# Performance work log

Hardware: AMD Instinct MI355X
Metric: run time of the kernel (lower is better)

The kernel has to match this reference:

```python
import jax, jax.numpy as jnp
import numpy as np

N, F = 4096, 255          # nodes, raw feature dim (one-hot adds +1 -> 256)
HID, D = 256, 256         # GCN hidden and out_dim
B, T, G = 8, 16384, 4     # n_breakings, n_tuples, n_groups
LN_EPS = 1e-5


def setup_inputs() -> dict:
    key = jax.random.key(0)
    ks = jax.random.split(key, 8)
    X = jax.random.normal(ks[0], (N, F), jnp.float32)
    adj_t = jax.random.uniform(ks[1], (N, N), jnp.float32)  # dense weighted adjacency
    W1 = jax.random.normal(ks[2], (F + 1, HID), jnp.float32) * 0.05
    b1 = jnp.zeros((HID,), jnp.float32)
    W2 = jax.random.normal(ks[3], (HID, D), jnp.float32) * 0.05
    b2 = jnp.zeros((D,), jnp.float32)
    ln_gamma = jnp.ones((D,), jnp.float32)
    ln_beta = jnp.zeros((D,), jnp.float32)
    tuples_coo = jax.random.randint(ks[4], (2, T), 0, N)
    group_idx = jax.random.randint(ks[5], (B,), 0, G)
    return dict(X=X, adj_t=adj_t, W1=W1, b1=b1, W2=W2, b2=b2,
                ln_gamma=ln_gamma, ln_beta=ln_beta,
                tuples_coo=tuples_coo, group_idx=group_idx,
                n_breakings=B, n_groups=G)


def reference(X, adj_t, W1, b1, W2, b2, ln_gamma, ln_beta,
              tuples_coo, group_idx, n_breakings, n_groups):
    n = X.shape[0]
    # --- symmetry breaking: top-k degree nodes (ties improbable for float degrees) ---
    deg = adj_t.sum(-1)                                   # [N]
    _, brk_idx = jax.lax.top_k(deg, n_breakings)          # [B]
    one_hot = jax.nn.one_hot(brk_idx, n, dtype=X.dtype)   # [B, N]
    # --- concat broadcast features with one-hot breaking channel ---
    Xin = jnp.concatenate(
        [jnp.broadcast_to(X[None], (n_breakings,) + X.shape), one_hot[..., None]],
        axis=-1)                                          # [B, N, F+1]
    # --- symmetry_breaking_model: 2-layer dense-adjacency GCN ---
    h = jax.nn.relu(jnp.einsum('nm,bmf->bnf', adj_t, Xin) @ W1 + b1)   # [B, N, HID]
    out = jnp.einsum('nm,bmf->bnf', adj_t, h) @ W2 + b2                # [B, N, D]
    # --- LayerNorm over feature dim ---
    mu = out.mean(-1, keepdims=True)
    var = out.var(-1, keepdims=True)
    holo = (out - mu) * jax.lax.rsqrt(var + LN_EPS) * ln_gamma + ln_beta  # [B, N, D]
    # --- gather tuple endpoints and reduce by product over arity ---
    gathered = holo[:, tuples_coo]                        # [B, arity, T, D]
    set_repr = gathered.prod(axis=1)                      # [B, T, D]
    # --- scatter-mean over breakings by group ---
    sums = jax.ops.segment_sum(set_repr, group_idx, num_segments=n_groups)  # [G, T, D]
    counts = jax.ops.segment_sum(jnp.ones((set_repr.shape[0],), set_repr.dtype),
                                 group_idx, num_segments=n_groups)          # [G]
    link = sums / jnp.maximum(counts, 1.0)[:, None, None]  # [G, T, D]
    # transpose(0,1).flatten(1,2): [T, G*D]
    return jnp.transpose(link, (1, 0, 2)).reshape(link.shape[1], -1)
```

## Files before the change

### kernel.cpp

```cpp
#include <hip/hip_runtime.h>
#include <hip/hip_bf16.h>

#define N_NODES 4096
#define FEAT    255
#define NB      8
#define NT      16384
#define NG      4

typedef __attribute__((ext_vector_type(8))) short          short8;
typedef __attribute__((ext_vector_type(8))) __bf16         bf16x8;
typedef __attribute__((ext_vector_type(4))) float          f32x4;
typedef __attribute__((ext_vector_type(4))) unsigned short ushort4v;

__device__ __forceinline__ unsigned short f2bf(float f) {
  unsigned int u = __builtin_bit_cast(unsigned int, f);
  u += 0x7fffu + ((u >> 16) & 1u);
  return (unsigned short)(u >> 16);
}

__device__ __forceinline__ f32x4 mfma16(short8 a, short8 b, f32x4 c) {
  return __builtin_amdgcn_mfma_f32_16x16x32_bf16(
      __builtin_bit_cast(bf16x8, a), __builtin_bit_cast(bf16x8, b), c, 0, 0, 0);
}

__device__ __forceinline__ void gload_lds16(const void* g, void* l) {
  __builtin_amdgcn_global_load_lds((__attribute__((address_space(1))) void*)(void*)g,
                                   (__attribute__((address_space(3))) void*)l, 16, 0, 0);
}

__global__ __launch_bounds__(256)
void deg_cvt(const float* __restrict__ adj, unsigned short* __restrict__ adjbf,
             float* __restrict__ deg)
{
  const int n = blockIdx.x;
  const int tid = threadIdx.x;
  const float* row = adj + (size_t)n * N_NODES;
  float s = 0.f;
#pragma unroll
  for (int it = 0; it < 4; ++it) {
    int idx = it * 1024 + tid * 4;
    float4 v = *(const float4*)(row + idx);
    s += (v.x + v.y) + (v.z + v.w);
    ushort4v o;
    o[0] = f2bf(v.x); o[1] = f2bf(v.y); o[2] = f2bf(v.z); o[3] = f2bf(v.w);
    *(ushort4v*)(adjbf + (size_t)n * N_NODES + idx) = o;
  }
#pragma unroll
  for (int off = 32; off > 0; off >>= 1) s += __shfl_xor(s, off);
  __shared__ float ws4[4];
  if ((tid & 63) == 0) ws4[tid >> 6] = s;
  __syncthreads();
  if (tid == 0) deg[n] = (ws4[0] + ws4[1]) + (ws4[2] + ws4[3]);
}

__global__ __launch_bounds__(256)
void topk_kernel(const float* __restrict__ deg, int* __restrict__ brk)
{
  __shared__ float v[N_NODES];
  __shared__ float wv[4];
  __shared__ int   wi[4];
  const int tid = threadIdx.x;
  for (int i = tid; i < N_NODES; i += 256) v[i] = deg[i];
  __syncthreads();
  for (int it = 0; it < NB; ++it) {
    float best = -1e30f; int bidx = 0x7fffffff;
#pragma unroll
    for (int k = 0; k < N_NODES / 256; ++k) {
      int i = k * 256 + tid;
      float x = v[i];
      if (x > best) { best = x; bidx = i; }
    }
#pragma unroll
    for (int off = 1; off < 64; off <<= 1) {
      float ov = __shfl_xor(best, off);
      int   oi = __shfl_xor(bidx, off);
      if (ov > best || (ov == best && oi < bidx)) { best = ov; bidx = oi; }
    }
    if ((tid & 63) == 0) { wv[tid >> 6] = best; wi[tid >> 6] = bidx; }
    __syncthreads();
    if (tid == 0) {
      float bb = wv[0]; int bbi = wi[0];
#pragma unroll
      for (int k = 1; k < 4; ++k)
        if (wv[k] > bb || (wv[k] == bb && wi[k] < bbi)) { bb = wv[k]; bbi = wi[k]; }
      brk[it] = bbi;
      v[bbi] = -1e30f;
    }
    __syncthreads();
  }
}

__global__ __launch_bounds__(256)
void extract_cols(const float* __restrict__ adj, const int* __restrict__ brk,
                  float* __restrict__ adjcol)
{
  const int n = blockIdx.x * 256 + threadIdx.x;
#pragma unroll
  for (int b = 0; b < NB; ++b)
    adjcol[b * N_NODES + n] = adj[(size_t)n * N_NODES + brk[b]];
}

#define G0R 8
__global__ __launch_bounds__(256)
void gemm0(const float* __restrict__ X, const float* __restrict__ W1,
           unsigned short* __restrict__ Yt)
{
  __shared__ float xr[G0R][256];
  const int tid = threadIdx.x;
  const int m0  = blockIdx.x * G0R;
  for (int i = tid; i < G0R * FEAT; i += 256) {
    int r = i / FEAT, c = i - r * FEAT;
    xr[r][c] = X[(size_t)(m0 + r) * FEAT + c];
  }
  __syncthreads();
  const int d = tid;
  float s[G0R] = {};
  for (int fq = 0; fq < 252; fq += 4) {
    float w0 = W1[(fq + 0) * 256 + d];
    float w1 = W1[(fq + 1) * 256 + d];
    float w2 = W1[(fq + 2) * 256 + d];
    float w3 = W1[(fq + 3) * 256 + d];
#pragma unroll
    for (int r = 0; r < G0R; ++r) {
      float4 x4 = *(const float4*)&xr[r][fq];
      s[r] = fmaf(x4.x, w0, s[r]);
      s[r] = fmaf(x4.y, w1, s[r]);
      s[r] = fmaf(x4.z, w2, s[r]);
      s[r] = fmaf(x4.w, w3, s[r]);
    }
  }
  for (int f = 252; f < FEAT; ++f) {
    float wv = W1[f * 256 + d];
#pragma unroll
    for (int r = 0; r < G0R; ++r) s[r] = fmaf(xr[r][f], wv, s[r]);
  }
#pragma unroll
  for (int r = 0; r < G0R; ++r)
    Yt[(size_t)d * N_NODES + m0 + r] = f2bf(s[r]);
}

__global__ __launch_bounds__(256)
void w2t_kernel(const float* __restrict__ W2, unsigned short* __restrict__ W2t)
{
  const int k = blockIdx.x, d = threadIdx.x;
  W2t[(size_t)d * 256 + k] = f2bf(W2[(size_t)k * 256 + d]);
}

template<int BM, int BN, int BK, int FM, int FN, bool OUTBF>
__global__ __launch_bounds__(256)
void gemm_bt(const unsigned short* __restrict__ A, const unsigned short* __restrict__ Bt,
             void* __restrict__ Cv, int M, int Nn, int K)
{
  static_assert(BK == 64, "staging/swizzle math assumes BK=64 (128 B = 8 chunks/row)");
  __shared__ unsigned short As[BM * BK];
  __shared__ unsigned short Bs[BN * BK];
  const int tid  = threadIdx.x;
  const int lane = tid & 63;
  const int w    = tid >> 6;
  const int wr   = w >> 1, wc = w & 1;
  const int lhi  = lane >> 4, llo = lane & 15;
  const int brow = blockIdx.x * BM;
  const int bcol = blockIdx.y * BN;
  const int Kper = K / gridDim.z;
  const int kbeg = blockIdx.z * Kper;

  f32x4 acc[FM][FN];
  const f32x4 z = {0.f, 0.f, 0.f, 0.f};
#pragma unroll
  for (int m = 0; m < FM; ++m)
#pragma unroll
    for (int n = 0; n < FN; ++n) acc[m][n] = z;

  for (int k0 = kbeg; k0 < kbeg + Kper; k0 += BK) {
    __syncthreads();
#pragma unroll
    for (int i = 0; i < (BM * BK * 2) / 4096; ++i) {
      int byte = i * 4096 + tid * 16;
      int row  = byte >> 7;
      int sc   = ((byte >> 4) & 7) ^ (row & 7);
      gload_lds16(A + (size_t)(brow + row) * K + k0 + sc * 8,
                  As + ((i * 4096 + w * 1024) >> 1));
    }
#pragma unroll
    for (int i = 0; i < (BN * BK * 2) / 4096; ++i) {
      int byte = i * 4096 + tid * 16;
      int row  = byte >> 7;
      int sc   = ((byte >> 4) & 7) ^ (row & 7);
      gload_lds16(Bt + (size_t)(bcol + row) * K + k0 + sc * 8,
                  Bs + ((i * 4096 + w * 1024) >> 1));
    }
    __syncthreads();
#pragma unroll
    for (int kk = 0; kk < BK; kk += 32) {
      short8 fa[FM], fb[FN];
#pragma unroll
      for (int m = 0; m < FM; ++m) {
        const int ar = wr * FM * 16 + m * 16 + llo;
        const int ac = ((kk >> 3) + lhi) ^ (ar & 7);
        fa[m] = *(const short8*)&As[ar * BK + ac * 8];
      }
#pragma unroll
      for (int n = 0; n < FN; ++n) {
        const int br = wc * FN * 16 + n * 16 + llo;
        const int bc = ((kk >> 3) + lhi) ^ (br & 7);
        fb[n] = *(const short8*)&Bs[br * BK + bc * 8];
      }
#pragma unroll
      for (int m = 0; m < FM; ++m)
#pragma unroll
        for (int n = 0; n < FN; ++n)
          acc[m][n] = mfma16(fa[m], fb[n], acc[m][n]);
    }
  }
#pragma unroll
  for (int m = 0; m < FM; ++m)
#pragma unroll
    for (int n = 0; n < FN; ++n) {
      const int r = brow + wr * FM * 16 + m * 16 + lhi * 4;
      const int c = bcol + wc * FN * 16 + n * 16 + llo;
      if constexpr (OUTBF) {
        unsigned short* cp = (unsigned short*)Cv + (size_t)blockIdx.z * M * Nn
                             + (size_t)r * Nn + c;
#pragma unroll
        for (int i = 0; i < 4; ++i) cp[(size_t)i * Nn] = f2bf(acc[m][n][i]);
      } else {
        float* cp = (float*)Cv + (size_t)blockIdx.z * M * Nn + (size_t)r * Nn + c;
#pragma unroll
        for (int i = 0; i < 4; ++i) cp[(size_t)i * Nn] = acc[m][n][i];
      }
    }
}

__global__ __launch_bounds__(256)
void reduce4(const float* __restrict__ bp, float* __restrict__ base)
{
  const size_t i = (size_t)blockIdx.x * 256 + threadIdx.x;
  const float4* b0 = (const float4*)bp;
  const float4* b1 = b0 + (size_t)N_NODES * 256 / 4;
  const float4* b2 = b1 + (size_t)N_NODES * 256 / 4;
  const float4* b3 = b2 + (size_t)N_NODES * 256 / 4;
  float4 v0 = b0[i], v1 = b1[i], v2 = b2[i], v3 = b3[i];
  float4 o;
  o.x = ((v0.x + v1.x) + v2.x) + v3.x;
  o.y = ((v0.y + v1.y) + v2.y) + v3.y;
  o.z = ((v0.z + v1.z) + v2.z) + v3.z;
  o.w = ((v0.w + v1.w) + v2.w) + v3.w;
  ((float4*)base)[i] = o;
}

__global__ __launch_bounds__(256)
void h_kernel(const float* __restrict__ base, const float* __restrict__ adjcol,
              const float* __restrict__ b1, const float* __restrict__ W1,
              unsigned short* __restrict__ Ht)
{
  __shared__ float bs[32][261];
  const int tid = threadIdx.x;
  const int m0  = blockIdx.x * 32;
  const int b   = blockIdx.y;
#pragma unroll
  for (int it = 0; it < 8; ++it) {
    int lin = it * 1024 + tid * 4;
    int mm = lin >> 8, d = lin & 255;
    float4 v = *(const float4*)(base + (size_t)(m0 + mm) * 256 + d);
    bs[mm][d] = v.x; bs[mm][d + 1] = v.y; bs[mm][d + 2] = v.z; bs[mm][d + 3] = v.w;
  }
  __syncthreads();
  const int ml = tid & 31, dg = tid >> 5;
  const float ac = adjcol[b * N_NODES + m0 + ml];
  const float* w1l = W1 + 255 * 256;
#pragma unroll 4
  for (int dd = 0; dd < 32; ++dd) {
    int d = dg * 32 + dd;
    float v = bs[ml][d] + b1[d] + ac * w1l[d];
    v = fmaxf(v, 0.f);
    Ht[(size_t)(b * 256 + d) * N_NODES + m0 + ml] = f2bf(v);
  }
}

__global__ __launch_bounds__(256)
void gemm3_ln(const unsigned short* __restrict__ Mcat, const unsigned short* __restrict__ W2t,
              const float* __restrict__ b2, const float* __restrict__ gamma,
              const float* __restrict__ beta, float* __restrict__ holo)
{
  const int tid  = threadIdx.x;
  const int w    = tid >> 6, lane = tid & 63;
  const int lhi  = lane >> 4, llo = lane & 15;
  const int n0   = blockIdx.x * 64;
  const int b    = blockIdx.y;
  const int row0 = n0 + w * 16;

  f32x4 acc[16];
  const f32x4 z = {0.f, 0.f, 0.f, 0.f};
#pragma unroll
  for (int j = 0; j < 16; ++j) acc[j] = z;

  const unsigned short* arow = Mcat + (size_t)(row0 + llo) * 2048 + b * 256;
#pragma unroll
  for (int k0 = 0; k0 < 256; k0 += 32) {
    const short8 fa = *(const short8*)&arow[k0 + lhi * 8];
#pragma unroll
    for (int j = 0; j < 16; ++j) {
      const short8 fb = *(const short8*)&W2t[(size_t)(j * 16 + llo) * 256 + k0 + lhi * 8];
      acc[j] = mfma16(fa, fb, acc[j]);
    }
  }
  float b2v[16];
#pragma unroll
  for (int j = 0; j < 16; ++j) b2v[j] = b2[j * 16 + llo];

  float mu[4], rs[4];
#pragma unroll
  for (int i = 0; i < 4; ++i) {
    float s = 0.f;
#pragma unroll
    for (int j = 0; j < 16; ++j) s += acc[j][i] + b2v[j];
    s += __shfl_xor(s, 1); s += __shfl_xor(s, 2);
    s += __shfl_xor(s, 4); s += __shfl_xor(s, 8);
    mu[i] = s * (1.f / 256.f);
  }
#pragma unroll
  for (int i = 0; i < 4; ++i) {
    float q = 0.f;
#pragma unroll
    for (int j = 0; j < 16; ++j) { float d = acc[j][i] + b2v[j] - mu[i]; q += d * d; }
    q += __shfl_xor(q, 1); q += __shfl_xor(q, 2);
    q += __shfl_xor(q, 4); q += __shfl_xor(q, 8);
    rs[i] = rsqrtf(q * (1.f / 256.f) + 1e-5f);
  }
  float* hb = holo + ((size_t)b * N_NODES + row0 + lhi * 4) * 256 + llo;
#pragma unroll
  for (int j = 0; j < 16; ++j) {
    const float gv = gamma[j * 16 + llo];
    const float bt = beta[j * 16 + llo];
#pragma unroll
    for (int i = 0; i < 4; ++i) {
      float x = acc[j][i] + b2v[j];
      hb[(size_t)i * 256 + j * 16] = (x - mu[i]) * rs[i] * gv + bt;
    }
  }
}

__global__ __launch_bounds__(256)
void gather_k(const float* __restrict__ holo, const int* __restrict__ tc,
              const int* __restrict__ gidx, float* __restrict__ out)
{
  const int t = blockIdx.x;
  const int d = threadIdx.x;
  const int i = tc[t];
  const int j = tc[NT + t];
  float a0 = 0.f, a1 = 0.f, a2 = 0.f, a3 = 0.f;
  float c0 = 0.f, c1 = 0.f, c2 = 0.f, c3 = 0.f;
#pragma unroll
  for (int b = 0; b < NB; ++b) {
    const int g = gidx[b];
    const float p = holo[((size_t)b * N_NODES + i) * 256 + d] *
                    holo[((size_t)b * N_NODES + j) * 256 + d];
    a0 += (g == 0) ? p : 0.f;  c0 += (g == 0) ? 1.f : 0.f;
    a1 += (g == 1) ? p : 0.f;  c1 += (g == 1) ? 1.f : 0.f;
    a2 += (g == 2) ? p : 0.f;  c2 += (g == 2) ? 1.f : 0.f;
    a3 += (g == 3) ? p : 0.f;  c3 += (g == 3) ? 1.f : 0.f;
  }
  float* ob = out + (size_t)t * 1024 + d;
  ob[0]   = a0 / fmaxf(c0, 1.f);
  ob[256] = a1 / fmaxf(c1, 1.f);
  ob[512] = a2 / fmaxf(c2, 1.f);
  ob[768] = a3 / fmaxf(c3, 1.f);
}

extern "C" void kernel_launch(void* const* d_in, const int* in_sizes, int n_in,
                              void* d_out, int out_size, void* d_ws, size_t ws_size,
                              hipStream_t stream)
{
  const float* X     = (const float*)d_in[0];
  const float* adj   = (const float*)d_in[1];
  const float* W1    = (const float*)d_in[2];
  const float* b1    = (const float*)d_in[3];
  const float* W2    = (const float*)d_in[4];
  const float* b2    = (const float*)d_in[5];
  const float* gamma = (const float*)d_in[6];
  const float* beta  = (const float*)d_in[7];
  const int*   tc    = (const int*)d_in[8];
  const int*   gidx  = (const int*)d_in[9];

  char* w = (char*)d_ws;
  size_t off = 0;
  unsigned short* adjbf = (unsigned short*)(w + off);
  float*          holo  = (float*)(w + off);  off += 33554432;
  unsigned short* Ht    = (unsigned short*)(w + off); off += 16777216;
  unsigned short* Mcat  = (unsigned short*)(w + off); off += 16777216;
  float*          basep = (float*)(w + off);  off += 16777216;
  float*          base  = (float*)(w + off);  off += 4194304;
  unsigned short* Yt    = (unsigned short*)(w + off); off += 2097152;
  float*          deg   = (float*)(w + off);  off += 16384;
  int*            brk   = (int*)(w + off);    off += 256;
  float*          adjcol= (float*)(w + off);  off += 131072;
  unsigned short* W2t   = (unsigned short*)(w + off); off += 131072;
  float* out = (float*)d_out;

  deg_cvt     <<<N_NODES, 256, 0, stream>>>(adj, adjbf, deg);
  topk_kernel <<<1, 256, 0, stream>>>(deg, brk);
  extract_cols<<<N_NODES / 256, 256, 0, stream>>>(adj, brk, adjcol);
  gemm0       <<<N_NODES / G0R, 256, 0, stream>>>(X, W1, Yt);
  w2t_kernel  <<<256, 256, 0, stream>>>(W2, W2t);
  gemm_bt<64, 64, 64, 2, 2, false><<<dim3(N_NODES / 64, 256 / 64, 4), 256, 0, stream>>>(
      adjbf, Yt, basep, N_NODES, 256, N_NODES);
  reduce4     <<<N_NODES * 256 / 4 / 256, 256, 0, stream>>>(basep, base);
  h_kernel    <<<dim3(N_NODES / 32, NB), 256, 0, stream>>>(base, adjcol, b1, W1, Ht);
  gemm_bt<128, 128, 64, 4, 4, true><<<dim3(N_NODES / 128, 2048 / 128, 1), 256, 0, stream>>>(
      adjbf, Ht, Mcat, N_NODES, 2048, N_NODES);
  gemm3_ln    <<<dim3(N_NODES / 64, NB), 256, 0, stream>>>(Mcat, W2t, b2, gamma, beta, holo);
  gather_k    <<<NT, 256, 0, stream>>>(holo, tc, gidx, out);
}
```

Measured before the change: 374.8 us.

## Fuse prep kernels, fold split-K reduce into h_kernel, interleave holo by node

Merges extract_cols, gemm0 and the W2 transpose into one prep kernel dispatched by block index, removing two launches. Drops the separate reduce4 pass: h_kernel now sums the four split-K partials directly while loading, so the 4 MB base buffer is never written and read back. Changes the holo layout to node-major with breakings interleaved, so gather_k reads 8 contiguous 1 KB rows per endpoint instead of 8 scattered rows. Also widens the first GEMM tile to 64x128, which halves its column blocks. The cost is 8x redundant reading of the partials across the breaking blocks in h_kernel, though these likely hit in cache.

Measured after the change: 362.6 us. -3.3%, faster.

```diff
diff --git a/kernel.cpp b/kernel.cpp
--- a/kernel.cpp
+++ b/kernel.cpp
@@ -90,60 +90,57 @@
   }
 }
 
-__global__ __launch_bounds__(256)
-void extract_cols(const float* __restrict__ adj, const int* __restrict__ brk,
-                  float* __restrict__ adjcol)
-{
-  const int n = blockIdx.x * 256 + threadIdx.x;
-#pragma unroll
-  for (int b = 0; b < NB; ++b)
-    adjcol[b * N_NODES + n] = adj[(size_t)n * N_NODES + brk[b]];
-}
-
 #define G0R 8
 __global__ __launch_bounds__(256)
-void gemm0(const float* __restrict__ X, const float* __restrict__ W1,
-           unsigned short* __restrict__ Yt)
+void prep_kernel(const float* __restrict__ X, const float* __restrict__ W1,
+                 const float* __restrict__ adj, const int* __restrict__ brk,
+                 const float* __restrict__ W2,
+                 unsigned short* __restrict__ Yt, float* __restrict__ adjcol,
+                 unsigned short* __restrict__ W2t)
 {
   __shared__ float xr[G0R][256];
+  const int bid = blockIdx.x;
   const int tid = threadIdx.x;
-  const int m0  = blockIdx.x * G0R;
-  for (int i = tid; i < G0R * FEAT; i += 256) {
-    int r = i / FEAT, c = i - r * FEAT;
-    xr[r][c] = X[(size_t)(m0 + r) * FEAT + c];
-  }
-  __syncthreads();
-  const int d = tid;
-  float s[G0R] = {};
-  for (int fq = 0; fq < 252; fq += 4) {
-    float w0 = W1[(fq + 0) * 256 + d];
-    float w1 = W1[(fq + 1) * 256 + d];
-    float w2 = W1[(fq + 2) * 256 + d];
-    float w3 = W1[(fq + 3) * 256 + d];
-#pragma unroll
-    for (int r = 0; r < G0R; ++r) {
-      float4 x4 = *(const float4*)&xr[r][fq];
-      s[r] = fmaf(x4.x, w0, s[r]);
-      s[r] = fmaf(x4.y, w1, s[r]);
-      s[r] = fmaf(x4.z, w2, s[r]);
-      s[r] = fmaf(x4.w, w3, s[r]);
-    }
-  }
-  for (int f = 252; f < FEAT; ++f) {
-    float wv = W1[f * 256 + d];
-#pragma unroll
-    for (int r = 0; r < G0R; ++r) s[r] = fmaf(xr[r][f], wv, s[r]);
-  }
-#pragma unroll
-  for (int r = 0; r < G0R; ++r)
-    Yt[(size_t)d * N_NODES + m0 + r] = f2bf(s[r]);
-}
-
-__global__ __launch_bounds__(256)
-void w2t_kernel(const float* __restrict__ W2, unsigned short* __restrict__ W2t)
-{
-  const int k = blockIdx.x, d = threadIdx.x;
-  W2t[(size_t)d * 256 + k] = f2bf(W2[(size_t)k * 256 + d]);
+  if (bid < 512) {
+    const int m0 = bid * G0R;
+    for (int i = tid; i < G0R * FEAT; i += 256) {
+      int r = i / FEAT, c = i - r * FEAT;
+      xr[r][c] = X[(size_t)(m0 + r) * FEAT + c];
+    }
+    __syncthreads();
+    const int d = tid;
+    float s[G0R] = {};
+    for (int fq = 0; fq < 252; fq += 4) {
+      float w0 = W1[(fq + 0) * 256 + d];
+      float w1 = W1[(fq + 1) * 256 + d];
+      float w2 = W1[(fq + 2) * 256 + d];
+      float w3 = W1[(fq + 3) * 256 + d];
+#pragma unroll
+      for (int r = 0; r < G0R; ++r) {
+        float4 x4 = *(const float4*)&xr[r][fq];
+        s[r] = fmaf(x4.x, w0, s[r]);
+        s[r] = fmaf(x4.y, w1, s[r]);
+        s[r] = fmaf(x4.z, w2, s[r]);
+        s[r] = fmaf(x4.w, w3, s[r]);
+      }
+    }
+    for (int f = 252; f < FEAT; ++f) {
+      float wv = W1[f * 256 + d];
+#pragma unroll
+      for (int r = 0; r < G0R; ++r) s[r] = fmaf(xr[r][f], wv, s[r]);
+    }
+#pragma unroll
+    for (int r = 0; r < G0R; ++r)
+      Yt[(size_t)d * N_NODES + m0 + r] = f2bf(s[r]);
+  } else if (bid < 528) {
+    const int n = (bid - 512) * 256 + tid;
+#pragma unroll
+    for (int b = 0; b < NB; ++b)
+      adjcol[b * N_NODES + n] = adj[(size_t)n * N_NODES + brk[b]];
+  } else {
+    const int k = bid - 528, d = tid;
+    W2t[(size_t)d * 256 + k] = f2bf(W2[(size_t)k * 256 + d]);
+  }
 }
 
 template<int BM, int BN, int BK, int FM, int FN, bool OUTBF>
@@ -152,6 +149,7 @@
              void* __restrict__ Cv, int M, int Nn, int K)
 {
   static_assert(BK == 64, "staging/swizzle math assumes BK=64 (128 B = 8 chunks/row)");
+  static_assert(BM == 2 * FM * 16 && BN == 2 * FN * 16, "2x2 wave grid");
   __shared__ unsigned short As[BM * BK];
   __shared__ unsigned short Bs[BN * BK];
   const int tid  = threadIdx.x;
@@ -232,24 +230,7 @@
 }
 
 __global__ __launch_bounds__(256)
-void reduce4(const float* __restrict__ bp, float* __restrict__ base)
-{
-  const size_t i = (size_t)blockIdx.x * 256 + threadIdx.x;
-  const float4* b0 = (const float4*)bp;
-  const float4* b1 = b0 + (size_t)N_NODES * 256 / 4;
-  const float4* b2 = b1 + (size_t)N_NODES * 256 / 4;
-  const float4* b3 = b2 + (size_t)N_NODES * 256 / 4;
-  float4 v0 = b0[i], v1 = b1[i], v2 = b2[i], v3 = b3[i];
-  float4 o;
-  o.x = ((v0.x + v1.x) + v2.x) + v3.x;
-  o.y = ((v0.y + v1.y) + v2.y) + v3.y;
-  o.z = ((v0.z + v1.z) + v2.z) + v3.z;
-  o.w = ((v0.w + v1.w) + v2.w) + v3.w;
-  ((float4*)base)[i] = o;
-}
-
-__global__ __launch_bounds__(256)
-void h_kernel(const float* __restrict__ base, const float* __restrict__ adjcol,
+void h_kernel(const float* __restrict__ basep, const float* __restrict__ adjcol,
               const float* __restrict__ b1, const float* __restrict__ W1,
               unsigned short* __restrict__ Ht)
 {
@@ -261,8 +242,15 @@
   for (int it = 0; it < 8; ++it) {
     int lin = it * 1024 + tid * 4;
     int mm = lin >> 8, d = lin & 255;
-    float4 v = *(const float4*)(base + (size_t)(m0 + mm) * 256 + d);
-    bs[mm][d] = v.x; bs[mm][d + 1] = v.y; bs[mm][d + 2] = v.z; bs[mm][d + 3] = v.w;
+    const float* p = basep + (size_t)(m0 + mm) * 256 + d;
+    float4 v0 = *(const float4*)(p);
+    float4 v1 = *(const float4*)(p + 1048576);
+    float4 v2 = *(const float4*)(p + 2097152);
+    float4 v3 = *(const float4*)(p + 3145728);
+    bs[mm][d]     = ((v0.x + v1.x) + v2.x) + v3.x;
+    bs[mm][d + 1] = ((v0.y + v1.y) + v2.y) + v3.y;
+    bs[mm][d + 2] = ((v0.z + v1.z) + v2.z) + v3.z;
+    bs[mm][d + 3] = ((v0.w + v1.w) + v2.w) + v3.w;
   }
   __syncthreads();
   const int ml = tid & 31, dg = tid >> 5;
@@ -327,7 +315,7 @@
     q += __shfl_xor(q, 4); q += __shfl_xor(q, 8);
     rs[i] = rsqrtf(q * (1.f / 256.f) + 1e-5f);
   }
-  float* hb = holo + ((size_t)b * N_NODES + row0 + lhi * 4) * 256 + llo;
+  float* hb = holo + ((size_t)(row0 + lhi * 4) * 8 + b) * 256 + llo;
 #pragma unroll
   for (int j = 0; j < 16; ++j) {
     const float gv = gamma[j * 16 + llo];
@@ -335,7 +323,7 @@
 #pragma unroll
     for (int i = 0; i < 4; ++i) {
       float x = acc[j][i] + b2v[j];
-      hb[(size_t)i * 256 + j * 16] = (x - mu[i]) * rs[i] * gv + bt;
+      hb[(size_t)i * 2048 + j * 16] = (x - mu[i]) * rs[i] * gv + bt;
     }
   }
 }
@@ -348,13 +336,14 @@
   const int d = threadIdx.x;
   const int i = tc[t];
   const int j = tc[NT + t];
+  const float* hi = holo + (size_t)i * 2048 + d;
+  const float* hj = holo + (size_t)j * 2048 + d;
   float a0 = 0.f, a1 = 0.f, a2 = 0.f, a3 = 0.f;
   float c0 = 0.f, c1 = 0.f, c2 = 0.f, c3 = 0.f;
 #pragma unroll
   for (int b = 0; b < NB; ++b) {
     const int g = gidx[b];
-    const float p = holo[((size_t)b * N_NODES + i) * 256 + d] *
-                    holo[((size_t)b * N_NODES + j) * 256 + d];
+    const float p = hi[b * 256] * hj[b * 256];
     a0 += (g == 0) ? p : 0.f;  c0 += (g == 0) ? 1.f : 0.f;
     a1 += (g == 1) ? p : 0.f;  c1 += (g == 1) ? 1.f : 0.f;
     a2 += (g == 2) ? p : 0.f;  c2 += (g == 2) ? 1.f : 0.f;
@@ -389,7 +378,6 @@
   unsigned short* Ht    = (unsigned short*)(w + off); off += 16777216;
   unsigned short* Mcat  = (unsigned short*)(w + off); off += 16777216;
   float*          basep = (float*)(w + off);  off += 16777216;
-  float*          base  = (float*)(w + off);  off += 4194304;
   unsigned short* Yt    = (unsigned short*)(w + off); off += 2097152;
   float*          deg   = (float*)(w + off);  off += 16384;
   int*            brk   = (int*)(w + off);    off += 256;
@@ -399,13 +387,10 @@
 
   deg_cvt     <<<N_NODES, 256, 0, stream>>>(adj, adjbf, deg);
   topk_kernel <<<1, 256, 0, stream>>>(deg, brk);
-  extract_cols<<<N_NODES / 256, 256, 0, stream>>>(adj, brk, adjcol);
-  gemm0       <<<N_NODES / G0R, 256, 0, stream>>>(X, W1, Yt);
-  w2t_kernel  <<<256, 256, 0, stream>>>(W2, W2t);
-  gemm_bt<64, 64, 64, 2, 2, false><<<dim3(N_NODES / 64, 256 / 64, 4), 256, 0, stream>>>(
+  prep_kernel <<<784, 256, 0, stream>>>(X, W1, adj, brk, W2, Yt, adjcol, W2t);
+  gemm_bt<64, 128, 64, 2, 4, false><<<dim3(N_NODES / 64, 256 / 128, 4), 256, 0, stream>>>(
       adjbf, Yt, basep, N_NODES, 256, N_NODES);
-  reduce4     <<<N_NODES * 256 / 4 / 256, 256, 0, stream>>>(basep, base);
-  h_kernel    <<<dim3(N_NODES / 32, NB), 256, 0, stream>>>(base, adjcol, b1, W1, Ht);
+  h_kernel    <<<dim3(N_NODES / 32, NB), 256, 0, stream>>>(basep, adjcol, b1, W1, Ht);
   gemm_bt<128, 128, 64, 4, 4, true><<<dim3(N_NODES / 128, 2048 / 128, 1), 256, 0, stream>>>(
       adjbf, Ht, Mcat, N_NODES, 2048, N_NODES);
   gemm3_ln    <<<dim3(N_NODES / 64, NB), 256, 0, stream>>>(Mcat, W2t, b2, gamma, beta, holo);
```
